# Performance work log

Measured on AMD Instinct MI355X. Metric: run time of the kernel, lower is better.

Reference implementation:

```python
import jax, jax.numpy as jnp
import numpy as np

B, C, L = 256, 512, 150
CI = C // 4            # channel_in = in_dim // 4 = 128
K = 150                # one_hot_cls_num (depthwise kernel over length)
POOL = 150             # MaxPool2d kernel (150, 1)
EPS = 1e-5             # BatchNorm eps


def setup_inputs() -> dict:
    key = jax.random.key(0)
    ks = jax.random.split(key, 8)
    n = lambda k, shape, s: jax.random.normal(k, shape, jnp.float32) * s
    return {
        "x":    jax.random.normal(ks[0], (B, C, L, 1), jnp.float32),
        "Wv":   n(ks[1], (CI, C), 0.06),   "bv": jnp.zeros((CI,), jnp.float32),
        "Wq":   n(ks[2], (CI, CI), 0.12),  "bq": jnp.zeros((CI,), jnp.float32),
        "Wk":   n(ks[3], (CI, CI), 0.12),  "bk": jnp.zeros((CI,), jnp.float32),
        "gamma": n(ks[4], (), 1.0),
        "Wd":   n(ks[5], (2 * CI, K), 0.1), "bd": jnp.zeros((2 * CI,), jnp.float32),
        "Wp":   n(ks[6], (2 * CI, 2 * CI), 0.08), "bp": jnp.zeros((2 * CI,), jnp.float32),
        "bn_g": jnp.ones((2 * CI,), jnp.float32),
        "bn_b": jnp.zeros((2 * CI,), jnp.float32),
    }


def reference(x, Wv, bv, Wq, bq, Wk, bk, gamma, Wd, bd, Wp, bp, bn_g, bn_b):
    xb = x[..., 0]                                             # [B, C, L] (trailing width==1)
    # 1x1 convs are per-position matmuls over the channel dim
    v = jnp.einsum('oc,bcl->bol', Wv, xb) + bv[:, None]        # [B, CI, L]
    q = jnp.einsum('oc,bcl->bol', Wq, v) + bq[:, None]         # [B, CI, L]
    k = jnp.einsum('oc,bcl->bol', Wk, v) + bk[:, None]         # [B, CI, L]
    # raw (unscaled) attention: energy = q^T k, softmax over keys
    energy = jnp.einsum('bci,bcj->bij', q, k)                  # [B, L, L]
    attn = jax.nn.softmax(energy, axis=-1)
    # x = bmm(v, attn^T): out[b,c,i] = sum_j v[b,c,j] * attn[b,i,j]
    att_out = jnp.einsum('bcj,bij->bci', v, attn)              # [B, CI, L]
    cat = jnp.concatenate([gamma * att_out, v], axis=1)        # [B, 2CI, L]
    # MaxPool2d kernel=(150,1), stride=(150,1) over length
    Lp = L // POOL
    y = cat[:, :, : Lp * POOL].reshape(B, 2 * CI, Lp, POOL).max(axis=-1)
    y = y.reshape(B, -1)                                       # [B, 2CI*Lp]
    # depthwise conv kernel (K,1), VALID padding, groups = 2CI
    dw = jax.lax.conv_general_dilated(
        cat[:, :, :, None],                                    # [B, 2CI, L, 1]
        Wd[:, None, :, None],                                  # [2CI, 1, K, 1]
        window_strides=(1, 1), padding='VALID',
        dimension_numbers=('NCHW', 'OIHW', 'NCHW'),
        feature_group_count=2 * CI,
    ) + bd[None, :, None, None]                                # [B, 2CI, L-K+1, 1]
    # pointwise 1x1 conv
    pw = jnp.einsum('oc,bchw->bohw', Wp, dw) + bp[None, :, None, None]
    # BatchNorm2d in training mode: per-channel batch stats (biased variance)
    mean = pw.mean(axis=(0, 2, 3))
    var = pw.var(axis=(0, 2, 3))
    xn = (pw - mean[None, :, None, None]) * jax.lax.rsqrt(var[None, :, None, None] + EPS)
    out = jax.nn.relu(xn * bn_g[None, :, None, None] + bn_b[None, :, None, None])
    return jnp.concatenate([out.reshape(B, -1), y], axis=1)    # [B, 2CI*(L-K+1) + 2CI*Lp]
```

## Files before the change

kernel.cpp:

```cpp
#include <hip/hip_runtime.h>


typedef float f32x4  __attribute__((ext_vector_type(4)));
typedef float f32x16 __attribute__((ext_vector_type(16)));
typedef short s16x8  __attribute__((ext_vector_type(8)));
typedef unsigned short BF;

union U8 { s16x8 v; BF u[8]; uint2 d[2]; unsigned w[4]; };

__device__ __forceinline__ BF bfhi(float f) { return (BF)(__float_as_uint(f) >> 16); }
__device__ __forceinline__ float bff(BF h) { return __uint_as_float(((unsigned)h) << 16); }
__device__ __forceinline__ BF bflo(float f, BF hi) { return bfhi(f - bff(hi)); }
__device__ __forceinline__ BF bfrne(float f) {
    unsigned u = __float_as_uint(f);
    u += 0x7fffu + ((u >> 16) & 1u);
    return (BF)(u >> 16);
}
__device__ __forceinline__ s16x8 ld8l(const BF* p) {
    U8 t; t.d[0] = *(const uint2*)p; t.d[1] = *(const uint2*)(p + 4); return t.v;
}
__device__ __forceinline__ void st4(BF* p, BF a, BF b, BF c, BF d) {
    uint2 t; t.x = (unsigned)a | ((unsigned)b << 16);
    t.y = (unsigned)c | ((unsigned)d << 16);
    *(uint2*)p = t;
}
__device__ __forceinline__ void ldv8(const unsigned* p, s16x8& hi, s16x8& lo) {
    unsigned u[8];
    *(uint4*)&u[0] = *(const uint4*)p;
    *(uint4*)&u[4] = *(const uint4*)(p + 4);
    U8 H, L;
    #pragma unroll
    for (int e = 0; e < 4; ++e) {
        unsigned a = u[2*e], b2 = u[2*e + 1];
        H.w[e] = (a >> 16) | (b2 & 0xffff0000u);
        L.w[e] = (a & 0xffffu) | (b2 << 16);
    }
    hi = H.v; lo = L.v;
}
#define MFMA(a, b, c)   __builtin_amdgcn_mfma_f32_16x16x32_bf16(a, b, c, 0, 0, 0)
#define MFMA32(a, b, c) __builtin_amdgcn_mfma_f32_32x32x16_bf16(a, b, c, 0, 0, 0)

__global__ __launch_bounds__(256)
void prep_all(const float* __restrict__ Wv, const float* __restrict__ Wq,
              const float* __restrict__ Wk, const float* __restrict__ bq,
              BF* __restrict__ wvh, BF* __restrict__ wvl,
              BF* __restrict__ wqh, BF* __restrict__ wql,
              float* __restrict__ cvec)
{
    __shared__ float qs[128][33], ks_[128][33];
    const int blk = blockIdx.x, tid = threadIdx.x;
    if (blk < 64) {
        int i = blk * 1024 + tid * 4;
        float4 v = *(const float4*)(Wv + i);
        BF h0 = bfhi(v.x), h1 = bfhi(v.y), h2 = bfhi(v.z), h3 = bfhi(v.w);
        st4(&wvh[i], h0, h1, h2, h3);
        st4(&wvl[i], bflo(v.x,h0), bflo(v.y,h1), bflo(v.z,h2), bflo(v.w,h3));
    } else if (blk < 80) {
        int bi = blk - 64;
        int d1_0 = (bi >> 2) * 32, d2_0 = (bi & 3) * 32;
        for (int i = tid; i < 4096; i += 256) {
            int o = i >> 5, c = i & 31;
            qs[o][c]  = Wq[o * 128 + d1_0 + c];
            ks_[o][c] = Wk[o * 128 + d2_0 + c];
        }
        __syncthreads();
        #pragma unroll
        for (int j = 0; j < 4; ++j) {
            int idx = j * 256 + tid;
            int d1 = idx >> 5, d2 = idx & 31;
            float s = 0.f;
            #pragma unroll 8
            for (int o = 0; o < 128; ++o) s = fmaf(qs[o][d1], ks_[o][d2], s);
            BF h = bfhi(s);
            wqh[(d1_0 + d1) * 128 + d2_0 + d2] = h;
            wql[(d1_0 + d1) * 128 + d2_0 + d2] = bflo(s, h);
        }
    } else {
        if (tid < 128) {
            float s = 0.f;
            for (int o = 0; o < 128; ++o) s += bq[o] * Wk[o * 128 + tid];
            cvec[tid] = s;
        }
    }
}

__global__ __launch_bounds__(512, 4)
void k1_v(const float* __restrict__ x, const BF* __restrict__ wvh,
          const BF* __restrict__ wvl, const float* __restrict__ bv,
          const float* __restrict__ Wd,
          unsigned* __restrict__ vp, float* __restrict__ vpm,
          float* __restrict__ vpd)
{
    __shared__ BF xt[2][2][80][36];
    const int bx = blockIdx.x;
    const int b = bx & 255, lh = bx >> 8;
    const int l0 = lh * 80;
    const float* xb = x + (long)b * 76800 + l0;
    const int tid = threadIdx.x, lane = tid & 63, w = tid >> 6;
    const int li = lane & 15, gq = lane >> 4;

    if (w < 4) {
        f32x4 acc[5][2];
        #pragma unroll
        for (int mf = 0; mf < 5; ++mf)
            #pragma unroll
            for (int nf = 0; nf < 2; ++nf) acc[mf][nf] = f32x4{0.f,0.f,0.f,0.f};
        s16x8 bh[2], bl[2];
        #pragma unroll
        for (int nf = 0; nf < 2; ++nf) {
            long g = (long)(w*32 + nf*16 + li)*512 + gq*8;
            bh[nf] = *(const s16x8*)(wvh + g);
            bl[nf] = *(const s16x8*)(wvl + g);
        }
        __syncthreads();
        for (int p = 0; p < 16; ++p) {
            s16x8 nbh[2], nbl[2];
            if (p < 15) {
                #pragma unroll
                for (int nf = 0; nf < 2; ++nf) {
                    long g = (long)(w*32 + nf*16 + li)*512 + (p+1)*32 + gq*8;
                    nbh[nf] = *(const s16x8*)(wvh + g);
                    nbl[nf] = *(const s16x8*)(wvl + g);
                }
            }
            const BF (*xh)[36] = xt[p & 1][0];
            const BF (*xl)[36] = xt[p & 1][1];
            #pragma unroll
            for (int mf = 0; mf < 5; ++mf) {
                int row = mf*16 + li;
                s16x8 ah = ld8l(&xh[row][gq*8]);
                s16x8 al = ld8l(&xl[row][gq*8]);
                #pragma unroll
                for (int nf = 0; nf < 2; ++nf) {
                    acc[mf][nf] = MFMA(al, bh[nf], acc[mf][nf]);
                    acc[mf][nf] = MFMA(ah, bl[nf], acc[mf][nf]);
                    acc[mf][nf] = MFMA(ah, bh[nf], acc[mf][nf]);
                }
            }
            if (p < 15) {
                #pragma unroll
                for (int nf = 0; nf < 2; ++nf) { bh[nf] = nbh[nf]; bl[nf] = nbl[nf]; }
            }
            __syncthreads();
        }
        #pragma unroll
        for (int nf = 0; nf < 2; ++nf) {
            int c = w*32 + nf*16 + li;
            float bvv = bv[c];
            float mx = -3.4e38f, dt = 0.f;
            #pragma unroll
            for (int mf = 0; mf < 5; ++mf)
                #pragma unroll
                for (int r = 0; r < 4; ++r) {
                    int ll = mf*16 + gq*4 + r;
                    float f = acc[mf][nf][r] + bvv;
                    BF h = bfhi(f);
                    BF lo2 = bflo(f, h);
                    vp[((long)b*160 + l0 + ll)*128 + c] = ((unsigned)h << 16) | lo2;
                    if (l0 + ll < 150) {
                        mx = fmaxf(mx, f);
                        dt = fmaf(f, Wd[(128 + c)*150 + l0 + ll], dt);
                    }
                }
            mx = fmaxf(mx, __shfl_xor(mx, 16)); dt += __shfl_xor(dt, 16);
            mx = fmaxf(mx, __shfl_xor(mx, 32)); dt += __shfl_xor(dt, 32);
            if (gq == 0) {
                vpm[((long)lh*256 + b)*128 + c] = mx;
                vpd[((long)lh*256 + b)*128 + c] = dt;
            }
        }
    } else {
        const int sw = w - 4;
        const int bound = (lh == 0) ? 16 : 6;
        float cur[2][8];
        auto ldchunk = [&](int p) {
            #pragma unroll
            for (int cc = 0; cc < 8; ++cc) {
                int ch = p*32 + sw*8 + cc;
                cur[0][cc] = xb[ch*150 + lane];
                cur[1][cc] = (lane < bound) ? xb[ch*150 + 64 + lane] : 0.f;
            }
        };
        auto wrchunk = [&](int buf) {
            #pragma unroll
            for (int g2 = 0; g2 < 2; ++g2) {
                BF h0 = bfhi(cur[0][g2*4+0]), h1 = bfhi(cur[0][g2*4+1]);
                BF h2 = bfhi(cur[0][g2*4+2]), h3 = bfhi(cur[0][g2*4+3]);
                st4(&xt[buf][0][lane][sw*8 + g2*4], h0, h1, h2, h3);
                st4(&xt[buf][1][lane][sw*8 + g2*4],
                    bflo(cur[0][g2*4+0],h0), bflo(cur[0][g2*4+1],h1),
                    bflo(cur[0][g2*4+2],h2), bflo(cur[0][g2*4+3],h3));
                if (lane < 16) {
                    BF k0 = bfhi(cur[1][g2*4+0]), k1 = bfhi(cur[1][g2*4+1]);
                    BF k2 = bfhi(cur[1][g2*4+2]), k3 = bfhi(cur[1][g2*4+3]);
                    st4(&xt[buf][0][64 + lane][sw*8 + g2*4], k0, k1, k2, k3);
                    st4(&xt[buf][1][64 + lane][sw*8 + g2*4],
                        bflo(cur[1][g2*4+0],k0), bflo(cur[1][g2*4+1],k1),
                        bflo(cur[1][g2*4+2],k2), bflo(cur[1][g2*4+3],k3));
                }
            }
        };
        ldchunk(0); wrchunk(0); ldchunk(1);
        __syncthreads();
        for (int p = 0; p < 16; ++p) {
            if (p < 15) {
                wrchunk((p + 1) & 1);
                if (p < 14) ldchunk(p + 2);
            }
            __syncthreads();
        }
    }
}

__global__ __launch_bounds__(1024, 8)
void k2_attn(const unsigned* __restrict__ vp,
             const BF* __restrict__ wqh, const BF* __restrict__ wql,
             const float* __restrict__ cvec, const float* __restrict__ gammap,
             const float* __restrict__ Wd,
             const float* __restrict__ vpm, const float* __restrict__ vpd,
             float* __restrict__ dw, float* __restrict__ out)
{
    __shared__ char smem[60672];
    BF (*ts)[2][192][36] = (BF(*)[2][192][36])smem;
    BF (*P)[172] = (BF(*)[172])smem;
    float* smax = (float*)(smem + 55296);
    float* ssum = smax + 480;
    float* svp  = ssum + 480;

    const int b = blockIdx.x;
    const unsigned* vb = vp + (long)b * 20480;
    const int tid = threadIdx.x;
    const int lane = tid & 63, w = tid >> 6;
    const int li = lane & 15, gq = lane >> 4;
    const int l31 = lane & 31, hi5 = lane >> 5;
    const float gamma = gammap[0];

    f32x4 eacc[2][4];
    #pragma unroll
    for (int a = 0; a < 2; ++a)
        #pragma unroll
        for (int b2 = 0; b2 < 4; ++b2) eacc[a][b2] = f32x4{0.f,0.f,0.f,0.f};
    const int iw = w / 3, jw = w % 3;

    for (int pr = 0; pr < 2; ++pr) {
        if (w < 10) {
            const int s2 = w / 5, jt = w % 5;
            const int ss = pr*2 + s2;
            f32x16 tacc;
            #pragma unroll
            for (int r = 0; r < 16; ++r) tacc[r] = 0.f;
            const unsigned* arow = vb + (jt*32 + l31)*128;
            const long brow = (long)(ss*32 + l31)*128;
            #pragma unroll
            for (int kc = 0; kc < 8; ++kc) {
                int kof = kc*16 + hi5*8;
                s16x8 bh = *(const s16x8*)(wqh + brow + kof);
                s16x8 bl = *(const s16x8*)(wql + brow + kof);
                s16x8 ah, al;
                ldv8(arow + kof, ah, al);
                tacc = MFMA32(al, bh, tacc);
                tacc = MFMA32(ah, bl, tacc);
                tacc = MFMA32(ah, bh, tacc);
            }
            #pragma unroll
            for (int r = 0; r < 16; ++r) {
                int j = jt*32 + (r & 3) + 8*(r >> 2) + 4*hi5;
                float f = tacc[r];
                BF h = bfhi(f);
                ts[s2][0][j][l31] = h;
                ts[s2][1][j][l31] = bflo(f, h);
            }
        } else if (pr == 0) {
            int t2 = tid - 640;
            unsigned* tz = (unsigned*)smem;
            for (int z = t2; z < 2304; z += 384) {
                int sb = z / 576, rz = z % 576;
                tz[(sb*192 + 160)*18 + rz] = 0u;
            }
            int r = t2 >> 1, hf = t2 & 1;
            if (r < 160) {
                const unsigned* vr = vb + r*128 + hf*64;
                float s = 0.f;
                #pragma unroll 8
                for (int d2 = 0; d2 < 64; ++d2)
                    s += cvec[hf*64 + d2] * bff((BF)(vr[d2] >> 16));
                svp[hf*192 + r] = s;
            }
        }
        __syncthreads();
        if (w < 15) {
            #pragma unroll
            for (int s2 = 0; s2 < 2; ++s2) {
                int scol = (pr*2 + s2)*32 + gq*8;
                s16x8 ah[2], al[2];
                #pragma unroll
                for (int mf2 = 0; mf2 < 2; ++mf2)
                    ldv8(vb + (iw*32 + mf2*16 + li)*128 + scol, ah[mf2], al[mf2]);
                #pragma unroll
                for (int nf = 0; nf < 4; ++nf) {
                    int jr = jw*64 + nf*16 + li;
                    s16x8 bh = ld8l(&ts[s2][0][jr][gq*8]);
                    s16x8 bl = ld8l(&ts[s2][1][jr][gq*8]);
                    #pragma unroll
                    for (int mf2 = 0; mf2 < 2; ++mf2) {
                        eacc[mf2][nf] = MFMA(ah[mf2], bh, eacc[mf2][nf]);
                        eacc[mf2][nf] = MFMA(ah[mf2], bl, eacc[mf2][nf]);
                        eacc[mf2][nf] = MFMA(al[mf2], bh, eacc[mf2][nf]);
                    }
                }
            }
        }
        __syncthreads();
    }

    if (w < 15) {
        #pragma unroll
        for (int nf = 0; nf < 4; ++nf) {
            int j = jw*64 + nf*16 + li;
            float sv = svp[j] + svp[192 + j];
            #pragma unroll
            for (int mf2 = 0; mf2 < 2; ++mf2)
                #pragma unroll
                for (int r = 0; r < 4; ++r)
                    eacc[mf2][nf][r] += sv;
        }
        #pragma unroll
        for (int mf2 = 0; mf2 < 2; ++mf2)
            #pragma unroll
            for (int r = 0; r < 4; ++r) {
                int i = iw*32 + mf2*16 + gq*4 + r;
                float m = -3.4e38f;
                #pragma unroll
                for (int nf = 0; nf < 4; ++nf) {
                    int j = jw*64 + nf*16 + li;
                    if (j < 150) m = fmaxf(m, eacc[mf2][nf][r]);
                }
                #pragma unroll
                for (int o = 1; o < 16; o <<= 1) m = fmaxf(m, __shfl_xor(m, o));
                if (li == 0) smax[jw*160 + i] = m;
            }
    }
    __syncthreads();
    if (w < 15) {
        #pragma unroll
        for (int mf2 = 0; mf2 < 2; ++mf2)
            #pragma unroll
            for (int r = 0; r < 4; ++r) {
                int i = iw*32 + mf2*16 + gq*4 + r;
                float gm = fmaxf(fmaxf(smax[i], smax[160 + i]), smax[320 + i]);
                float rs_ = 0.f;
                #pragma unroll
                for (int nf = 0; nf < 4; ++nf) {
                    int j = jw*64 + nf*16 + li;
                    float e = (j < 150) ? __expf(eacc[mf2][nf][r] - gm) : 0.f;
                    eacc[mf2][nf][r] = e;
                    rs_ += e;
                }
                #pragma unroll
                for (int o = 1; o < 16; o <<= 1) rs_ += __shfl_xor(rs_, o);
                if (li == 0) ssum[jw*160 + i] = rs_;
            }
    }
    __syncthreads();
    if (w < 15) {
        #pragma unroll
        for (int mf2 = 0; mf2 < 2; ++mf2)
            #pragma unroll
            for (int r = 0; r < 4; ++r) {
                int i = iw*32 + mf2*16 + gq*4 + r;
                float inv = 1.f / (ssum[i] + ssum[160 + i] + ssum[320 + i]);
                #pragma unroll
                for (int nf = 0; nf < 4; ++nf) {
                    int j = jw*64 + nf*16 + li;
                    if (j < 160) P[i][j] = bfrne(eacc[mf2][nf][r] * inv);
                }
            }
    }
    __syncthreads();

    {
        const int pc = w & 7, pi = w >> 3;
        f32x4 oacc[5];
        #pragma unroll
        for (int i = 0; i < 5; ++i) oacc[i] = f32x4{0.f,0.f,0.f,0.f};
        #pragma unroll
        for (int ks = 0; ks < 5; ++ks) {
            int c = pc*16 + li;
            int j0 = ks*32 + gq*8;
            U8 t;
            #pragma unroll
            for (int e = 0; e < 8; ++e)
                t.u[e] = (BF)(vb[(j0 + e)*128 + c] >> 16);
            #pragma unroll
            for (int nf2 = 0; nf2 < 5; ++nf2) {
                int ir = pi*80 + nf2*16 + li;
                s16x8 bp = ld8l(&P[ir][ks*32 + gq*8]);
                oacc[nf2] = MFMA(t.v, bp, oacc[nf2]);
            }
        }

        float* pmax = smax;
        float* pdot = ssum;
        #pragma unroll
        for (int r = 0; r < 4; ++r) {
            int c = pc*16 + gq*4 + r;
            float mx = -3.4e38f, dt = 0.f;
            #pragma unroll
            for (int nf2 = 0; nf2 < 5; ++nf2) {
                int l = pi*80 + nf2*16 + li;
                if (l < 150) {
                    float val = gamma * oacc[nf2][r];
                    mx = fmaxf(mx, val);
                    dt = fmaf(val, Wd[c*150 + l], dt);
                }
            }
            #pragma unroll
            for (int o = 1; o < 16; o <<= 1) {
                mx = fmaxf(mx, __shfl_xor(mx, o));
                dt += __shfl_xor(dt, o);
            }
            if (li == 0) { pmax[pi*128 + c] = mx; pdot[pi*128 + c] = dt; }
        }
        __syncthreads();
        if (tid < 128) {
            out[(long)b*512 + 256 + tid] = fmaxf(pmax[tid], pmax[128 + tid]);
            dw[b*256 + tid] = pdot[tid] + pdot[128 + tid];
        } else if (tid < 256) {
            int c2 = tid - 128;
            float m0 = vpm[(long)b*128 + c2];
            float m1 = vpm[(long)(256 + b)*128 + c2];
            out[(long)b*512 + 384 + c2] = fmaxf(m0, m1);
            dw[b*256 + 128 + c2] = vpd[(long)b*128 + c2] + vpd[(long)(256 + b)*128 + c2];
        }
    }
}

__global__ __launch_bounds__(256)
void tail_pwbn(const float* __restrict__ dw, const float* __restrict__ Wp,
               const float* __restrict__ bn_g, const float* __restrict__ bn_b,
               float* __restrict__ out)
{
    __shared__ float wp_s[256];
    __shared__ float rs[4], rs2[4];
    const int o = blockIdx.x, t = threadIdx.x;
    const int lane = t & 63, w = t >> 6;
    wp_s[t] = Wp[o * 256 + t];
    __syncthreads();
    const float4* dr = (const float4*)(dw + (long)t * 256);
    float acc = 0.f;
    #pragma unroll 8
    for (int i = 0; i < 64; ++i) {
        float4 d4 = dr[i];
        acc = fmaf(d4.x, wp_s[i*4+0], acc);
        acc = fmaf(d4.y, wp_s[i*4+1], acc);
        acc = fmaf(d4.z, wp_s[i*4+2], acc);
        acc = fmaf(d4.w, wp_s[i*4+3], acc);
    }
    float s = acc, s2 = acc * acc;
    #pragma unroll
    for (int d = 1; d < 64; d <<= 1) { s += __shfl_xor(s, d); s2 += __shfl_xor(s2, d); }
    if (lane == 0) { rs[w] = s; rs2[w] = s2; }
    __syncthreads();
    float S  = rs[0] + rs[1] + rs[2] + rs[3];
    float S2 = rs2[0] + rs2[1] + rs2[2] + rs2[3];
    float mean = S * (1.f/256.f);
    float var  = S2 * (1.f/256.f) - mean * mean;
    float sc = rsqrtf(var + 1e-5f) * bn_g[o];
    float sh = bn_b[o] - mean * sc;
    out[(long)t * 512 + o] = fmaxf(fmaf(acc, sc, sh), 0.f);
}

extern "C" void kernel_launch(void* const* d_in, const int* in_sizes, int n_in,
                              void* d_out, int out_size, void* d_ws, size_t ws_size,
                              hipStream_t stream)
{
    (void)in_sizes; (void)n_in; (void)out_size; (void)ws_size;
    const float* x    = (const float*)d_in[0];
    const float* Wv   = (const float*)d_in[1];
    const float* bv   = (const float*)d_in[2];
    const float* Wq   = (const float*)d_in[3];
    const float* bq   = (const float*)d_in[4];
    const float* Wk   = (const float*)d_in[5];
    const float* bk   = (const float*)d_in[6];  (void)bk;
    const float* gam  = (const float*)d_in[7];
    const float* Wd   = (const float*)d_in[8];
    const float* Wp   = (const float*)d_in[10];
    const float* bn_g = (const float*)d_in[12];
    const float* bn_b = (const float*)d_in[13];
    float* out = (float*)d_out;

    char* wsb = (char*)d_ws;
    BF* wvh   = (BF*)wsb;
    BF* wvl   = (BF*)(wsb + 131072);
    BF* wqh   = (BF*)(wsb + 262144);
    BF* wql   = (BF*)(wsb + 294912);
    float* cvec = (float*)(wsb + 327680);
    unsigned* vpck = (unsigned*)(wsb + 328192);
    float* vpm  = (float*)(wsb + 21299712);
    float* vpd  = (float*)(wsb + 21561856);
    float* dw   = (float*)wsb;

    prep_all<<<81, 256, 0, stream>>>(Wv, Wq, Wk, bq, wvh, wvl, wqh, wql, cvec);
    k1_v<<<512, 512, 0, stream>>>(x, wvh, wvl, bv, Wd, vpck, vpm, vpd);
    k2_attn<<<256, 1024, 0, stream>>>(vpck, wqh, wql, cvec, gam, Wd, vpm, vpd,
                                      dw, out);
    tail_pwbn<<<256, 256, 0, stream>>>(dw, Wp, bn_g, bn_b, out);
}
```

Before: 107.7 us.

## Move T=Wqk·v projection into k1 and split attention across query tiles

The projection T = (WqᵀWk)·v and the per-key bias term are now computed inside the v-projection kernel from its LDS-resident v tile and written to global memory. The attention kernel then works on 32-query slices, with 1280 blocks of 512 threads instead of 256 blocks of 1024, and streams T strips through double-buffered LDS. A new small kernel combines the per-slice max and depthwise-dot partials. This should raise parallelism and occupancy on the GPU, at the cost of an extra ~21MB global write and read of T, re-reading v per slice, and one more launch.

```diff
diff --git a/kernel.cpp b/kernel.cpp
--- a/kernel.cpp
+++ b/kernel.cpp
@@ -2,7 +2,6 @@
 
 
 typedef float f32x4  __attribute__((ext_vector_type(4)));
-typedef float f32x16 __attribute__((ext_vector_type(16)));
 typedef short s16x8  __attribute__((ext_vector_type(8)));
 typedef unsigned short BF;
 
@@ -37,8 +36,11 @@
     }
     hi = H.v; lo = L.v;
 }
-#define MFMA(a, b, c)   __builtin_amdgcn_mfma_f32_16x16x32_bf16(a, b, c, 0, 0, 0)
-#define MFMA32(a, b, c) __builtin_amdgcn_mfma_f32_32x32x16_bf16(a, b, c, 0, 0, 0)
+__device__ __forceinline__ unsigned packf(float f) {
+    BF h = bfhi(f);
+    return ((unsigned)h << 16) | (unsigned)bflo(f, h);
+}
+#define MFMA(a, b, c) __builtin_amdgcn_mfma_f32_16x16x32_bf16(a, b, c, 0, 0, 0)
 
 __global__ __launch_bounds__(256)
 void prep_all(const float* __restrict__ Wv, const float* __restrict__ Wq,
@@ -85,13 +87,18 @@
 }
 
 __global__ __launch_bounds__(512, 4)
-void k1_v(const float* __restrict__ x, const BF* __restrict__ wvh,
-          const BF* __restrict__ wvl, const float* __restrict__ bv,
-          const float* __restrict__ Wd,
-          unsigned* __restrict__ vp, float* __restrict__ vpm,
-          float* __restrict__ vpd)
+void k1_vt(const float* __restrict__ x, const BF* __restrict__ wvh,
+           const BF* __restrict__ wvl, const float* __restrict__ bv,
+           const BF* __restrict__ wqh, const BF* __restrict__ wql,
+           const float* __restrict__ cvec, const float* __restrict__ Wd,
+           unsigned* __restrict__ vp, unsigned* __restrict__ tT,
+           float* __restrict__ svg, float* __restrict__ vpm,
+           float* __restrict__ vpd)
 {
-    __shared__ BF xt[2][2][80][36];
+    __shared__ char smem[42240];
+    BF (*xt)[2][80][36] = (BF(*)[2][80][36])smem;
+    unsigned (*vpk)[132] = (unsigned(*)[132])smem;
+
     const int bx = blockIdx.x;
     const int b = bx & 255, lh = bx >> 8;
     const int l0 = lh * 80;
@@ -154,9 +161,9 @@
                 for (int r = 0; r < 4; ++r) {
                     int ll = mf*16 + gq*4 + r;
                     float f = acc[mf][nf][r] + bvv;
-                    BF h = bfhi(f);
-                    BF lo2 = bflo(f, h);
-                    vp[((long)b*160 + l0 + ll)*128 + c] = ((unsigned)h << 16) | lo2;
+                    unsigned pk = packf(f);
+                    vp[((long)b*160 + l0 + ll)*128 + c] = pk;
+                    vpk[ll][c] = pk;
                     if (l0 + ll < 150) {
                         mx = fmaxf(mx, f);
                         dt = fmaf(f, Wd[(128 + c)*150 + l0 + ll], dt);
@@ -210,204 +217,204 @@
             __syncthreads();
         }
     }
-}
-
-__global__ __launch_bounds__(1024, 8)
-void k2_attn(const unsigned* __restrict__ vp,
-             const BF* __restrict__ wqh, const BF* __restrict__ wql,
-             const float* __restrict__ cvec, const float* __restrict__ gammap,
+    __syncthreads();
+
+    if (tid < 160) {
+        int j = tid >> 1, hf = tid & 1;
+        float s = 0.f;
+        #pragma unroll 8
+        for (int d2 = hf*64; d2 < hf*64 + 64; ++d2)
+            s += cvec[d2] * bff((BF)(vpk[j][d2] >> 16));
+        s += __shfl_xor(s, 1);
+        if (hf == 0) svg[(long)b*160 + l0 + j] = s;
+    }
+
+    {
+        const int c0 = w * 16;
+        f32x4 acc2[5];
+        #pragma unroll
+        for (int i = 0; i < 5; ++i) acc2[i] = f32x4{0.f,0.f,0.f,0.f};
+        #pragma unroll
+        for (int kd = 0; kd < 4; ++kd) {
+            long ga = (long)(c0 + li)*128 + kd*32 + gq*8;
+            s16x8 ah = *(const s16x8*)(wqh + ga);
+            s16x8 al = *(const s16x8*)(wql + ga);
+            #pragma unroll
+            for (int jf = 0; jf < 5; ++jf) {
+                s16x8 vh_, vl_;
+                ldv8(&vpk[jf*16 + li][kd*32 + gq*8], vh_, vl_);
+                acc2[jf] = MFMA(ah, vl_, acc2[jf]);
+                acc2[jf] = MFMA(al, vh_, acc2[jf]);
+                acc2[jf] = MFMA(ah, vh_, acc2[jf]);
+            }
+        }
+        #pragma unroll
+        for (int jf = 0; jf < 5; ++jf) {
+            unsigned pk[4];
+            #pragma unroll
+            for (int r = 0; r < 4; ++r) pk[r] = packf(acc2[jf][r]);
+            *(uint4*)&tT[((long)b*160 + l0 + jf*16 + li)*128 + c0 + gq*4] = *(uint4*)pk;
+        }
+    }
+}
+
+__global__ __launch_bounds__(512, 4)
+void k2_attn(const unsigned* __restrict__ vp, const unsigned* __restrict__ tT,
+             const float* __restrict__ svg, const float* __restrict__ gammap,
              const float* __restrict__ Wd,
-             const float* __restrict__ vpm, const float* __restrict__ vpd,
-             float* __restrict__ dw, float* __restrict__ out)
+             float* __restrict__ pmax_g, float* __restrict__ pdot_g)
 {
-    __shared__ char smem[60672];
-    BF (*ts)[2][192][36] = (BF(*)[2][192][36])smem;
-    BF (*P)[172] = (BF(*)[172])smem;
-    float* smax = (float*)(smem + 55296);
-    float* ssum = smax + 480;
-    float* svp  = ssum + 480;
-
-    const int b = blockIdx.x;
+    __shared__ char smem[75008];
+    BF (*vAh)[132] = (BF(*)[132])smem;
+    BF (*vAl)[132] = (BF(*)[132])(smem + 8448);
+    unsigned (*tst)[160][36] = (unsigned(*)[160][36])(smem + 16896);
+    BF (*P)[172] = (BF(*)[172])(smem + 62976);
+    float* smax = (float*)(smem + 73984);
+    float* ssum = smax + 128;
+
+    const int bid = blockIdx.x;
+    const int b = bid & 255, i5 = bid >> 8;
+    const int i0 = i5 * 32;
     const unsigned* vb = vp + (long)b * 20480;
+    const unsigned* tb = tT + (long)b * 20480;
     const int tid = threadIdx.x;
     const int lane = tid & 63, w = tid >> 6;
     const int li = lane & 15, gq = lane >> 4;
-    const int l31 = lane & 31, hi5 = lane >> 5;
     const float gamma = gammap[0];
 
-    f32x4 eacc[2][4];
+    const int it = w >> 2, jw = w & 3;
+    const int jbase = (jw < 2) ? jw*48 : 96 + (jw - 2)*32;
+    const int nfcnt = (jw < 2) ? 3 : 2;
+
+    {
+        int row = tid >> 4, c8 = (tid & 15) * 8;
+        const unsigned* src = vb + ((long)(i0 + row))*128 + c8;
+        unsigned u[8];
+        *(uint4*)&u[0] = *(const uint4*)src;
+        *(uint4*)&u[4] = *(const uint4*)(src + 4);
+        BF hh[8], ll_[8];
+        #pragma unroll
+        for (int e = 0; e < 8; ++e) { hh[e] = (BF)(u[e] >> 16); ll_[e] = (BF)(u[e] & 0xffffu); }
+        st4(&vAh[row][c8], hh[0], hh[1], hh[2], hh[3]);
+        st4(&vAh[row][c8+4], hh[4], hh[5], hh[6], hh[7]);
+        st4(&vAl[row][c8], ll_[0], ll_[1], ll_[2], ll_[3]);
+        st4(&vAl[row][c8+4], ll_[4], ll_[5], ll_[6], ll_[7]);
+    }
+
+    uint4 sreg[4];
+    auto ldstrip = [&](int s) {
+        if (tid < 320) {
+            int j = tid >> 1, h = tid & 1;
+            const uint4* src = (const uint4*)(tb + (long)j*128 + s*32 + h*16);
+            sreg[0] = src[0]; sreg[1] = src[1]; sreg[2] = src[2]; sreg[3] = src[3];
+        }
+    };
+    auto wrstrip = [&](int buf) {
+        if (tid < 320) {
+            int j = tid >> 1, h = tid & 1;
+            unsigned* dst = &tst[buf][j][h*16];
+            *(uint4*)(dst + 0)  = sreg[0];
+            *(uint4*)(dst + 4)  = sreg[1];
+            *(uint4*)(dst + 8)  = sreg[2];
+            *(uint4*)(dst + 12) = sreg[3];
+        }
+    };
+
+    f32x4 eacc[3];
     #pragma unroll
-    for (int a = 0; a < 2; ++a)
-        #pragma unroll
-        for (int b2 = 0; b2 < 4; ++b2) eacc[a][b2] = f32x4{0.f,0.f,0.f,0.f};
-    const int iw = w / 3, jw = w % 3;
-
-    for (int pr = 0; pr < 2; ++pr) {
-        if (w < 10) {
-            const int s2 = w / 5, jt = w % 5;
-            const int ss = pr*2 + s2;
-            f32x16 tacc;
-            #pragma unroll
-            for (int r = 0; r < 16; ++r) tacc[r] = 0.f;
-            const unsigned* arow = vb + (jt*32 + l31)*128;
-            const long brow = (long)(ss*32 + l31)*128;
-            #pragma unroll
-            for (int kc = 0; kc < 8; ++kc) {
-                int kof = kc*16 + hi5*8;
-                s16x8 bh = *(const s16x8*)(wqh + brow + kof);
-                s16x8 bl = *(const s16x8*)(wql + brow + kof);
-                s16x8 ah, al;
-                ldv8(arow + kof, ah, al);
-                tacc = MFMA32(al, bh, tacc);
-                tacc = MFMA32(ah, bl, tacc);
-                tacc = MFMA32(ah, bh, tacc);
-            }
-            #pragma unroll
-            for (int r = 0; r < 16; ++r) {
-                int j = jt*32 + (r & 3) + 8*(r >> 2) + 4*hi5;
-                float f = tacc[r];
-                BF h = bfhi(f);
-                ts[s2][0][j][l31] = h;
-                ts[s2][1][j][l31] = bflo(f, h);
-            }
-        } else if (pr == 0) {
-            int t2 = tid - 640;
-            unsigned* tz = (unsigned*)smem;
-            for (int z = t2; z < 2304; z += 384) {
-                int sb = z / 576, rz = z % 576;
-                tz[(sb*192 + 160)*18 + rz] = 0u;
-            }
-            int r = t2 >> 1, hf = t2 & 1;
-            if (r < 160) {
-                const unsigned* vr = vb + r*128 + hf*64;
-                float s = 0.f;
-                #pragma unroll 8
-                for (int d2 = 0; d2 < 64; ++d2)
-                    s += cvec[hf*64 + d2] * bff((BF)(vr[d2] >> 16));
-                svp[hf*192 + r] = s;
-            }
+    for (int i = 0; i < 3; ++i) eacc[i] = f32x4{0.f,0.f,0.f,0.f};
+
+    ldstrip(0); wrstrip(0); ldstrip(1);
+    __syncthreads();
+
+    for (int s = 0; s < 4; ++s) {
+        if (s < 3) wrstrip((s + 1) & 1);
+        if (s < 2) ldstrip(s + 2);
+        const int buf = s & 1;
+        s16x8 ah = ld8l(&vAh[it*16 + li][s*32 + gq*8]);
+        s16x8 al = ld8l(&vAl[it*16 + li][s*32 + gq*8]);
+        for (int nf = 0; nf < nfcnt; ++nf) {
+            int jr = jbase + nf*16 + li;
+            s16x8 bh, bl;
+            ldv8(&tst[buf][jr][gq*8], bh, bl);
+            eacc[nf] = MFMA(ah, bl, eacc[nf]);
+            eacc[nf] = MFMA(al, bh, eacc[nf]);
+            eacc[nf] = MFMA(ah, bh, eacc[nf]);
         }
         __syncthreads();
-        if (w < 15) {
-            #pragma unroll
-            for (int s2 = 0; s2 < 2; ++s2) {
-                int scol = (pr*2 + s2)*32 + gq*8;
-                s16x8 ah[2], al[2];
-                #pragma unroll
-                for (int mf2 = 0; mf2 < 2; ++mf2)
-                    ldv8(vb + (iw*32 + mf2*16 + li)*128 + scol, ah[mf2], al[mf2]);
-                #pragma unroll
-                for (int nf = 0; nf < 4; ++nf) {
-                    int jr = jw*64 + nf*16 + li;
-                    s16x8 bh = ld8l(&ts[s2][0][jr][gq*8]);
-                    s16x8 bl = ld8l(&ts[s2][1][jr][gq*8]);
-                    #pragma unroll
-                    for (int mf2 = 0; mf2 < 2; ++mf2) {
-                        eacc[mf2][nf] = MFMA(ah[mf2], bh, eacc[mf2][nf]);
-                        eacc[mf2][nf] = MFMA(ah[mf2], bl, eacc[mf2][nf]);
-                        eacc[mf2][nf] = MFMA(al[mf2], bh, eacc[mf2][nf]);
-                    }
-                }
-            }
-        }
-        __syncthreads();
-    }
-
-    if (w < 15) {
-        #pragma unroll
-        for (int nf = 0; nf < 4; ++nf) {
-            int j = jw*64 + nf*16 + li;
-            float sv = svp[j] + svp[192 + j];
-            #pragma unroll
-            for (int mf2 = 0; mf2 < 2; ++mf2)
-                #pragma unroll
-                for (int r = 0; r < 4; ++r)
-                    eacc[mf2][nf][r] += sv;
-        }
-        #pragma unroll
-        for (int mf2 = 0; mf2 < 2; ++mf2)
-            #pragma unroll
-            for (int r = 0; r < 4; ++r) {
-                int i = iw*32 + mf2*16 + gq*4 + r;
-                float m = -3.4e38f;
-                #pragma unroll
-                for (int nf = 0; nf < 4; ++nf) {
-                    int j = jw*64 + nf*16 + li;
-                    if (j < 150) m = fmaxf(m, eacc[mf2][nf][r]);
-                }
-                #pragma unroll
-                for (int o = 1; o < 16; o <<= 1) m = fmaxf(m, __shfl_xor(m, o));
-                if (li == 0) smax[jw*160 + i] = m;
-            }
-    }
-    __syncthreads();
-    if (w < 15) {
-        #pragma unroll
-        for (int mf2 = 0; mf2 < 2; ++mf2)
-            #pragma unroll
-            for (int r = 0; r < 4; ++r) {
-                int i = iw*32 + mf2*16 + gq*4 + r;
-                float gm = fmaxf(fmaxf(smax[i], smax[160 + i]), smax[320 + i]);
-                float rs_ = 0.f;
-                #pragma unroll
-                for (int nf = 0; nf < 4; ++nf) {
-                    int j = jw*64 + nf*16 + li;
-                    float e = (j < 150) ? __expf(eacc[mf2][nf][r] - gm) : 0.f;
-                    eacc[mf2][nf][r] = e;
-                    rs_ += e;
-                }
-                #pragma unroll
-                for (int o = 1; o < 16; o <<= 1) rs_ += __shfl_xor(rs_, o);
-                if (li == 0) ssum[jw*160 + i] = rs_;
-            }
-    }
-    __syncthreads();
-    if (w < 15) {
-        #pragma unroll
-        for (int mf2 = 0; mf2 < 2; ++mf2)
-            #pragma unroll
-            for (int r = 0; r < 4; ++r) {
-                int i = iw*32 + mf2*16 + gq*4 + r;
-                float inv = 1.f / (ssum[i] + ssum[160 + i] + ssum[320 + i]);
-                #pragma unroll
-                for (int nf = 0; nf < 4; ++nf) {
-                    int j = jw*64 + nf*16 + li;
-                    if (j < 160) P[i][j] = bfrne(eacc[mf2][nf][r] * inv);
-                }
-            }
+    }
+
+    for (int nf = 0; nf < nfcnt; ++nf) {
+        int j = jbase + nf*16 + li;
+        float sv = svg[(long)b*160 + j];
+        #pragma unroll
+        for (int r = 0; r < 4; ++r) eacc[nf][r] += sv;
+    }
+    #pragma unroll
+    for (int r = 0; r < 4; ++r) {
+        int iloc = it*16 + gq*4 + r;
+        float m = -3.4e38f;
+        for (int nf = 0; nf < nfcnt; ++nf) {
+            int j = jbase + nf*16 + li;
+            if (j < 150) m = fmaxf(m, eacc[nf][r]);
+        }
+        #pragma unroll
+        for (int o = 1; o < 16; o <<= 1) m = fmaxf(m, __shfl_xor(m, o));
+        if (li == 0) smax[jw*32 + iloc] = m;
+    }
+    __syncthreads();
+    #pragma unroll
+    for (int r = 0; r < 4; ++r) {
+        int iloc = it*16 + gq*4 + r;
+        float gm = fmaxf(fmaxf(smax[iloc], smax[32 + iloc]),
+                         fmaxf(smax[64 + iloc], smax[96 + iloc]));
+        float rs_ = 0.f;
+        for (int nf = 0; nf < nfcnt; ++nf) {
+            int j = jbase + nf*16 + li;
+            float e = (j < 150) ? __expf(eacc[nf][r] - gm) : 0.f;
+            eacc[nf][r] = e;
+            rs_ += e;
+        }
+        #pragma unroll
+        for (int o = 1; o < 16; o <<= 1) rs_ += __shfl_xor(rs_, o);
+        if (li == 0) ssum[jw*32 + iloc] = rs_;
+    }
+    __syncthreads();
+    #pragma unroll
+    for (int r = 0; r < 4; ++r) {
+        int iloc = it*16 + gq*4 + r;
+        float inv = 1.f / (ssum[iloc] + ssum[32 + iloc] + ssum[64 + iloc] + ssum[96 + iloc]);
+        for (int nf = 0; nf < nfcnt; ++nf) {
+            int j = jbase + nf*16 + li;
+            P[iloc][j] = bfrne(eacc[nf][r] * inv);
+        }
     }
     __syncthreads();
 
     {
-        const int pc = w & 7, pi = w >> 3;
-        f32x4 oacc[5];
-        #pragma unroll
-        for (int i = 0; i < 5; ++i) oacc[i] = f32x4{0.f,0.f,0.f,0.f};
+        const int pc = w;
+        f32x4 oacc[2];
+        oacc[0] = f32x4{0.f,0.f,0.f,0.f};
+        oacc[1] = f32x4{0.f,0.f,0.f,0.f};
         #pragma unroll
         for (int ks = 0; ks < 5; ++ks) {
-            int c = pc*16 + li;
-            int j0 = ks*32 + gq*8;
             U8 t;
             #pragma unroll
             for (int e = 0; e < 8; ++e)
-                t.u[e] = (BF)(vb[(j0 + e)*128 + c] >> 16);
-            #pragma unroll
-            for (int nf2 = 0; nf2 < 5; ++nf2) {
-                int ir = pi*80 + nf2*16 + li;
-                s16x8 bp = ld8l(&P[ir][ks*32 + gq*8]);
+                t.u[e] = (BF)(vb[((long)(ks*32 + gq*8 + e))*128 + pc*16 + li] >> 16);
+            #pragma unroll
+            for (int nf2 = 0; nf2 < 2; ++nf2) {
+                s16x8 bp = ld8l(&P[nf2*16 + li][ks*32 + gq*8]);
                 oacc[nf2] = MFMA(t.v, bp, oacc[nf2]);
             }
         }
-
-        float* pmax = smax;
-        float* pdot = ssum;
         #pragma unroll
         for (int r = 0; r < 4; ++r) {
             int c = pc*16 + gq*4 + r;
             float mx = -3.4e38f, dt = 0.f;
             #pragma unroll
-            for (int nf2 = 0; nf2 < 5; ++nf2) {
-                int l = pi*80 + nf2*16 + li;
+            for (int nf2 = 0; nf2 < 2; ++nf2) {
+                int l = i0 + nf2*16 + li;
                 if (l < 150) {
                     float val = gamma * oacc[nf2][r];
                     mx = fmaxf(mx, val);
@@ -419,19 +426,34 @@
                 mx = fmaxf(mx, __shfl_xor(mx, o));
                 dt += __shfl_xor(dt, o);
             }
-            if (li == 0) { pmax[pi*128 + c] = mx; pdot[pi*128 + c] = dt; }
-        }
-        __syncthreads();
-        if (tid < 128) {
-            out[(long)b*512 + 256 + tid] = fmaxf(pmax[tid], pmax[128 + tid]);
-            dw[b*256 + tid] = pdot[tid] + pdot[128 + tid];
-        } else if (tid < 256) {
-            int c2 = tid - 128;
-            float m0 = vpm[(long)b*128 + c2];
-            float m1 = vpm[(long)(256 + b)*128 + c2];
-            out[(long)b*512 + 384 + c2] = fmaxf(m0, m1);
-            dw[b*256 + 128 + c2] = vpd[(long)b*128 + c2] + vpd[(long)(256 + b)*128 + c2];
-        }
+            if (li == 0) {
+                pmax_g[((long)i5*256 + b)*128 + c] = mx;
+                pdot_g[((long)i5*256 + b)*128 + c] = dt;
+            }
+        }
+    }
+}
+
+__global__ __launch_bounds__(256)
+void tail_comb(const float* __restrict__ pmax_g, const float* __restrict__ pdot_g,
+               const float* __restrict__ vpm, const float* __restrict__ vpd,
+               float* __restrict__ dw, float* __restrict__ out)
+{
+    const int b = blockIdx.x, ch = threadIdx.x;
+    if (ch < 128) {
+        float mx = -3.4e38f, dt = 0.f;
+        #pragma unroll
+        for (int i5 = 0; i5 < 5; ++i5) {
+            mx = fmaxf(mx, pmax_g[((long)i5*256 + b)*128 + ch]);
+            dt += pdot_g[((long)i5*256 + b)*128 + ch];
+        }
+        out[(long)b*512 + 256 + ch] = mx;
+        dw[b*256 + ch] = dt;
+    } else {
+        int c2 = ch - 128;
+        float m0 = vpm[(long)b*128 + c2], m1 = vpm[(long)(256 + b)*128 + c2];
+        out[(long)b*512 + 256 + ch] = fmaxf(m0, m1);
+        dw[b*256 + ch] = vpd[(long)b*128 + c2] + vpd[(long)(256 + b)*128 + c2];
     }
 }
 
@@ -496,13 +518,18 @@
     BF* wql   = (BF*)(wsb + 294912);
     float* cvec = (float*)(wsb + 327680);
     unsigned* vpck = (unsigned*)(wsb + 328192);
-    float* vpm  = (float*)(wsb + 21299712);
-    float* vpd  = (float*)(wsb + 21561856);
-    float* dw   = (float*)wsb;
+    unsigned* tT   = (unsigned*)(wsb + 21299712);
+    float* svg  = (float*)(wsb + 42271232);
+    float* vpm  = (float*)(wsb + 42435072);
+    float* vpd  = (float*)(wsb + 42697216);
+    float* pmax_g = (float*)(wsb + 42959360);
+    float* pdot_g = (float*)(wsb + 43614720);
+    float* dw   = (float*)(wsb + 44270080);
 
     prep_all<<<81, 256, 0, stream>>>(Wv, Wq, Wk, bq, wvh, wvl, wqh, wql, cvec);
-    k1_v<<<512, 512, 0, stream>>>(x, wvh, wvl, bv, Wd, vpck, vpm, vpd);
-    k2_attn<<<256, 1024, 0, stream>>>(vpck, wqh, wql, cvec, gam, Wd, vpm, vpd,
-                                      dw, out);
+    k1_vt<<<512, 512, 0, stream>>>(x, wvh, wvl, bv, wqh, wql, cvec, Wd,
+                                   vpck, tT, svg, vpm, vpd);
+    k2_attn<<<1280, 512, 0, stream>>>(vpck, tT, svg, gam, Wd, pmax_g, pdot_g);
+    tail_comb<<<256, 256, 0, stream>>>(pmax_g, pdot_g, vpm, vpd, dw, out);
     tail_pwbn<<<256, 256, 0, stream>>>(dw, Wp, bn_g, bn_b, out);
 }
```

Measured after the change: 124.2 us. 15.4% more time.
